# Optimization experiments

Measured on AMD Instinct MI355X. Metric: run time of the kernel, lower is better.

The kernel has to match this reference:

```python
import jax, jax.numpy as jnp
import numpy as np

H = 2048      # hidden_size
F = 1408      # moe_intermediate_size
E = 8         # num_experts
K = 2         # num_activated_experts
B, S = 4, 1024


def setup_inputs() -> dict:
    key = jax.random.key(0)
    ks = jax.random.split(key, 9)
    sc = 0.02
    return {
        "hidden_states": jax.random.normal(ks[0], (B, S, H), dtype=jnp.float32),
        "gate_w": jax.random.normal(ks[1], (E, H), dtype=jnp.float32) * sc,
        "bias": jnp.zeros((E,), dtype=jnp.float32),
        # shared expert (num_shared_experts = 1); torch Linear weight layout [out, in]
        "ws1": jax.random.normal(ks[2], (F, H), dtype=jnp.float32) * sc,
        "ws2": jax.random.normal(ks[3], (H, F), dtype=jnp.float32) * sc,
        "ws3": jax.random.normal(ks[4], (F, H), dtype=jnp.float32) * sc,
        # routed experts stacked along leading E axis
        "we1": jax.random.normal(ks[5], (E, F, H), dtype=jnp.float32) * sc,
        "we2": jax.random.normal(ks[6], (E, H, F), dtype=jnp.float32) * sc,
        "we3": jax.random.normal(ks[7], (E, F, H), dtype=jnp.float32) * sc,
    }


def reference(hidden_states, gate_w, bias, ws1, ws2, ws3, we1, we2, we3):
    orig_shape = hidden_states.shape
    x = hidden_states.reshape(-1, orig_shape[-1])      # [T, H]
    T = x.shape[0]

    # shared expert (SwiGLU)
    shared = (jax.nn.silu(x @ ws1.T) * (x @ ws3.T)) @ ws2.T   # [T, H]

    # sigmoid gating with bias-adjusted top-k selection
    scores = jax.nn.sigmoid(x @ gate_w.T)              # [T, E]
    routing_scores = scores + bias
    _, topk_idx = jax.lax.top_k(routing_scores, K)     # [T, K]
    sel = jnp.take_along_axis(scores, topk_idx, axis=1)
    gates = sel / sel.sum(axis=-1, keepdims=True)      # [T, K]

    # dense combine weights c[t, e] (top-k indices are distinct per token)
    c = jnp.zeros((T, E), dtype=x.dtype).at[jnp.arange(T)[:, None], topk_idx].add(gates)

    # all-expert SwiGLU, combined with sparse gate weights
    h1 = jnp.einsum("th,efh->etf", x, we1)             # [E, T, F]
    h3 = jnp.einsum("th,efh->etf", x, we3)
    act = jax.nn.silu(h1) * h3
    routed = jnp.einsum("etf,ehf,te->th", act, we2, c) # [T, H]

    return (shared + routed).reshape(orig_shape)
```

## Files before the change

kernel.cpp:

```cpp
#include <hip/hip_runtime.h>
#include <cstdint>
#include <cstddef>

#define TDIM 4096
#define HDIM 2048
#define FDIM 1408
#define NEXP 8
#define NSLOT (TDIM * 2)
#define BK 32

typedef _Float16 half8 __attribute__((ext_vector_type(8)));
typedef _Float16 half4 __attribute__((ext_vector_type(4)));
typedef float floatx4 __attribute__((ext_vector_type(4)));

#define AS1 __attribute__((address_space(1)))
#define AS3 __attribute__((address_space(3)))

__device__ __forceinline__ void g2l16(const _Float16* g, _Float16* l) {
  __builtin_amdgcn_global_load_lds((const AS1 unsigned*)g, (AS3 unsigned*)l, 16, 0, 0);
}

static constexpr size_t ws_align(size_t x) { return (x + 511) & ~(size_t)511; }
static constexpr size_t WS_XB     = 0;
static constexpr size_t WS_ACT_S  = WS_XB    + (size_t)TDIM * HDIM * 2;
static constexpr size_t WS_ACT_R  = WS_ACT_S + (size_t)TDIM * FDIM * 2;
static constexpr size_t WS_TOKE   = WS_ACT_R + (size_t)NSLOT * FDIM * 2;
static constexpr size_t WS_TOKG   = WS_TOKE  + (size_t)TDIM * 2 * 4;
static constexpr size_t WS_SLOTT  = WS_TOKG  + (size_t)TDIM * 2 * 4;
static constexpr size_t WS_SLOTG  = WS_SLOTT + (size_t)NSLOT * 4;
static constexpr size_t WS_COUNTS = WS_SLOTG + (size_t)NSLOT * 4;
static constexpr size_t WS_FILL   = WS_COUNTS + 64;
static constexpr size_t WS_OFFS   = WS_FILL   + 64;
static constexpr size_t WS_WS1H   = ws_align(WS_OFFS + 64);
static constexpr size_t WS_WS3H   = WS_WS1H + (size_t)FDIM * HDIM * 2;
static constexpr size_t WS_WS2H   = WS_WS3H + (size_t)FDIM * HDIM * 2;
static constexpr size_t WS_WE1H   = WS_WS2H + (size_t)HDIM * FDIM * 2;
static constexpr size_t WS_WE3H   = WS_WE1H + (size_t)NEXP * FDIM * HDIM * 2;
static constexpr size_t WS_WE2H   = WS_WE3H + (size_t)NEXP * FDIM * HDIM * 2;
static constexpr size_t WS_END    = WS_WE2H + (size_t)NEXP * HDIM * FDIM * 2;


__global__ void zero_meta_kernel(int* __restrict__ counts) {
  if (threadIdx.x < 32) counts[threadIdx.x] = 0;
}

__global__ void cvt3_kernel(const float* __restrict__ s0, const float* __restrict__ s1,
                            const float* __restrict__ s2, _Float16* __restrict__ d0,
                            _Float16* __restrict__ d1, _Float16* __restrict__ d2) {
  const float* s;
  _Float16* d;
  if (blockIdx.y == 0)      { s = s0; d = d0; }
  else if (blockIdx.y == 1) { s = s1; d = d1; }
  else                      { s = s2; d = d2; }
  size_t i = ((size_t)blockIdx.x * 256 + threadIdx.x) * 8;
  float4 a = *(const float4*)(s + i);
  float4 b = *(const float4*)(s + i + 4);
  half8 h;
  h[0] = (_Float16)a.x; h[1] = (_Float16)a.y; h[2] = (_Float16)a.z; h[3] = (_Float16)a.w;
  h[4] = (_Float16)b.x; h[5] = (_Float16)b.y; h[6] = (_Float16)b.z; h[7] = (_Float16)b.w;
  *(half8*)(d + i) = h;
}

__global__ void gate_kernel(const float* __restrict__ x, const float* __restrict__ gw,
                            const float* __restrict__ bias, _Float16* __restrict__ xb,
                            int* __restrict__ toke, float* __restrict__ tokg,
                            int* __restrict__ counts) {
  const int wid  = blockIdx.x * 4 + (threadIdx.x >> 6);
  const int lane = threadIdx.x & 63;
  const float4* xv = (const float4*)(x + (size_t)wid * HDIM);
  const float4* gv = (const float4*)gw;
  _Float16* xrow = xb + (size_t)wid * HDIM;
  float acc[NEXP];
#pragma unroll
  for (int e = 0; e < NEXP; ++e) acc[e] = 0.f;
#pragma unroll
  for (int i = 0; i < 8; ++i) {
    float4 xq = xv[lane + 64 * i];
    half4 hq;
    hq[0] = (_Float16)xq.x; hq[1] = (_Float16)xq.y;
    hq[2] = (_Float16)xq.z; hq[3] = (_Float16)xq.w;
    *(half4*)(xrow + 4 * (lane + 64 * i)) = hq;
#pragma unroll
    for (int e = 0; e < NEXP; ++e) {
      float4 gq = gv[e * 512 + lane + 64 * i];
      acc[e] += xq.x * gq.x + xq.y * gq.y + xq.z * gq.z + xq.w * gq.w;
    }
  }
#pragma unroll
  for (int e = 0; e < NEXP; ++e) {
    float v = acc[e];
    for (int off = 32; off; off >>= 1) v += __shfl_xor(v, off);
    acc[e] = v;
  }
  if (lane == 0) {
    float s[NEXP], r[NEXP];
#pragma unroll
    for (int e = 0; e < NEXP; ++e) {
      s[e] = 1.f / (1.f + __expf(-acc[e]));
      r[e] = s[e] + bias[e];
    }
    int e0 = 0;
#pragma unroll
    for (int e = 1; e < NEXP; ++e) if (r[e] > r[e0]) e0 = e;
    int e1 = -1;
#pragma unroll
    for (int e = 0; e < NEXP; ++e) if (e != e0 && (e1 < 0 || r[e] > r[e1])) e1 = e;
    float g0 = s[e0], g1 = s[e1];
    float inv = 1.f / (g0 + g1);
    toke[wid * 2]     = e0;
    toke[wid * 2 + 1] = e1;
    tokg[wid * 2]     = g0 * inv;
    tokg[wid * 2 + 1] = g1 * inv;
    atomicAdd(&counts[e0], 1);
    atomicAdd(&counts[e1], 1);
  }
}

__global__ void offsets_kernel(const int* __restrict__ counts, int* __restrict__ offs) {
  if (threadIdx.x == 0) {
    int o = 0;
    for (int e = 0; e < NEXP; ++e) { offs[e] = o; o += counts[e]; }
  }
}

__global__ void scatter_kernel(const int* __restrict__ toke, const float* __restrict__ tokg,
                               const int* __restrict__ offs, int* __restrict__ fill,
                               int* __restrict__ slott, float* __restrict__ slotg) {
  int t = blockIdx.x * 256 + threadIdx.x;
#pragma unroll
  for (int j = 0; j < 2; ++j) {
    int e = toke[t * 2 + j];
    float g = tokg[t * 2 + j];
    int p = offs[e] + atomicAdd(&fill[e], 1);
    slott[p] = t;
    slotg[p] = g;
  }
}


__global__ __launch_bounds__(256) void up_kernel(
    const _Float16* __restrict__ xb,
    const _Float16* __restrict__ ws1h, const _Float16* __restrict__ ws3h,
    const _Float16* __restrict__ we1h, const _Float16* __restrict__ we3h,
    _Float16* __restrict__ acts, _Float16* __restrict__ actr,
    const int* __restrict__ counts, const int* __restrict__ offs,
    const int* __restrict__ slott) {
  constexpr int GX = FDIM / 128;
  constexpr int GY = TDIM / 128;
  const int orig = blockIdx.x + GX * (blockIdx.y + GY * blockIdx.z);
  const int k8 = orig & 7, s = orig >> 3;
  const int g = k8 + 8 * (s / GX);
  const int lid = g * GX + (s % GX);
  const int bx = lid % GX;
  const int by = (lid / GX) % GY;
  const int bz = lid / (GX * GY);

  int cnt = TDIM, base = 0;
  const _Float16* __restrict__ W1 = ws1h;
  const _Float16* __restrict__ W3 = ws3h;
  _Float16* __restrict__ act = acts;
  bool gather = false;
  if (bz > 0) {
    const int e = bz - 1;
    cnt = counts[e];
    base = offs[e];
    if ((int)(by * 128) >= cnt) return;
    W1 = we1h + (size_t)e * FDIM * HDIM;
    W3 = we3h + (size_t)e * FDIM * HDIM;
    act = actr;
    gather = true;
  }
  const int m0 = by * 128, n0 = bx * 128;

  __shared__ _Float16 As[2][128 * BK];
  __shared__ _Float16 B1s[2][128 * BK];
  __shared__ _Float16 B3s[2][128 * BK];

  const int tid = threadIdx.x, lane = tid & 63, wv = tid >> 6;
  const int wm = wv >> 1, wn = wv & 1;
  const int lrow = lane & 15, quad = lane >> 4;

  const _Float16 *srcA[2], *srcB1[2], *srcB3[2];
#pragma unroll
  for (int j = 0; j < 2; ++j) {
    const int rr = wv * 32 + j * 16 + (lane >> 2);
    const int gc = ((lane & 3) ^ ((rr >> 1) & 3)) * 8;
    const int m = m0 + rr;
    int tok;
    if (gather) tok = slott[base + (m < cnt ? m : cnt - 1)];
    else tok = m;
    srcA[j]  = xb + (size_t)tok * HDIM + gc;
    srcB1[j] = W1 + (size_t)(n0 + rr) * HDIM + gc;
    srcB3[j] = W3 + (size_t)(n0 + rr) * HDIM + gc;
  }

  floatx4 acc1[4][4] = {};
  floatx4 acc3[4][4] = {};
  const int cA = (quad ^ ((lrow >> 1) & 3)) * 8;

#pragma unroll
  for (int j = 0; j < 2; ++j) {
    const int lb = (wv * 32 + j * 16) * BK;
    g2l16(srcA[j],  &As[0][lb]);
    g2l16(srcB1[j], &B1s[0][lb]);
    g2l16(srcB3[j], &B3s[0][lb]);
  }
  __syncthreads();

  for (int t = 0; t < HDIM / BK; ++t) {
    const int cur = t & 1;
    if (t + 1 < HDIM / BK) {
      const int k0 = (t + 1) * BK;
#pragma unroll
      for (int j = 0; j < 2; ++j) {
        const int lb = (wv * 32 + j * 16) * BK;
        g2l16(srcA[j] + k0,  &As[cur ^ 1][lb]);
        g2l16(srcB1[j] + k0, &B1s[cur ^ 1][lb]);
        g2l16(srcB3[j] + k0, &B3s[cur ^ 1][lb]);
      }
    }
    half8 af[4], b1f[4], b3f[4];
#pragma unroll
    for (int i = 0; i < 4; ++i)
      af[i] = *(const half8*)&As[cur][(wm * 64 + i * 16 + lrow) * BK + cA];
#pragma unroll
    for (int i = 0; i < 4; ++i) {
      b1f[i] = *(const half8*)&B1s[cur][(wn * 64 + i * 16 + lrow) * BK + cA];
      b3f[i] = *(const half8*)&B3s[cur][(wn * 64 + i * 16 + lrow) * BK + cA];
    }
#pragma unroll
    for (int ms = 0; ms < 4; ++ms)
#pragma unroll
      for (int ns = 0; ns < 4; ++ns) {
        acc1[ms][ns] = __builtin_amdgcn_mfma_f32_16x16x32_f16(af[ms], b1f[ns], acc1[ms][ns], 0, 0, 0);
        acc3[ms][ns] = __builtin_amdgcn_mfma_f32_16x16x32_f16(af[ms], b3f[ns], acc3[ms][ns], 0, 0, 0);
      }
    __syncthreads();
  }

#pragma unroll
  for (int ms = 0; ms < 4; ++ms)
#pragma unroll
    for (int ns = 0; ns < 4; ++ns)
#pragma unroll
      for (int r = 0; r < 4; ++r) {
        float h1 = acc1[ms][ns][r];
        float h3 = acc3[ms][ns][r];
        float a = h1 / (1.f + __expf(-h1)) * h3;
        const int rl = wm * 64 + ms * 16 + quad * 4 + r;
        const int f = n0 + wn * 64 + ns * 16 + lrow;
        const int m = m0 + rl;
        if (gather) {
          if (m < cnt) act[(size_t)(base + m) * FDIM + f] = (_Float16)a;
        } else {
          act[(size_t)m * FDIM + f] = (_Float16)a;
        }
      }
}

__global__ __launch_bounds__(256) void down_kernel(
    const _Float16* __restrict__ acts, const _Float16* __restrict__ actr,
    const _Float16* __restrict__ ws2h, const _Float16* __restrict__ we2h,
    float* __restrict__ out,
    const int* __restrict__ counts, const int* __restrict__ offs,
    const int* __restrict__ slott, const float* __restrict__ slotg) {
  constexpr int GX = HDIM / 128;
  constexpr int GY = TDIM / 128;
  const int orig = blockIdx.x + GX * (blockIdx.y + GY * blockIdx.z);
  const int k8 = orig & 7, s = orig >> 3;
  const int g = k8 + 8 * (s / GX);
  const int lid = g * GX + (s % GX);
  const int bx = lid % GX;
  const int by = (lid / GX) % GY;
  const int bz = lid / (GX * GY);

  int cnt = TDIM, base = 0;
  const _Float16* __restrict__ A = acts;
  const _Float16* __restrict__ W = ws2h;
  bool gather = false;
  if (bz > 0) {
    const int e = bz - 1;
    cnt = counts[e];
    base = offs[e];
    if ((int)(by * 128) >= cnt) return;
    A = actr;
    W = we2h + (size_t)e * HDIM * FDIM;
    gather = true;
  }
  const int m0 = by * 128, n0 = bx * 128;

  __shared__ _Float16 As[2][128 * BK];
  __shared__ _Float16 Bs[2][128 * BK];

  const int tid = threadIdx.x, lane = tid & 63, wv = tid >> 6;
  const int wm = wv >> 1, wn = wv & 1;
  const int lrow = lane & 15, quad = lane >> 4;

  const _Float16 *srcA[2], *srcB[2];
#pragma unroll
  for (int j = 0; j < 2; ++j) {
    const int rr = wv * 32 + j * 16 + (lane >> 2);
    const int gc = ((lane & 3) ^ ((rr >> 1) & 3)) * 8;
    const int m = m0 + rr;
    int srow;
    if (gather) srow = base + (m < cnt ? m : cnt - 1);
    else srow = m;
    srcA[j] = A + (size_t)srow * FDIM + gc;
    srcB[j] = W + (size_t)(n0 + rr) * FDIM + gc;
  }

  floatx4 acc[4][4] = {};
  const int cA = (quad ^ ((lrow >> 1) & 3)) * 8;

#pragma unroll
  for (int j = 0; j < 2; ++j) {
    const int lb = (wv * 32 + j * 16) * BK;
    g2l16(srcA[j], &As[0][lb]);
    g2l16(srcB[j], &Bs[0][lb]);
  }
  __syncthreads();

  for (int t = 0; t < FDIM / BK; ++t) {
    const int cur = t & 1;
    if (t + 1 < FDIM / BK) {
      const int k0 = (t + 1) * BK;
#pragma unroll
      for (int j = 0; j < 2; ++j) {
        const int lb = (wv * 32 + j * 16) * BK;
        g2l16(srcA[j] + k0, &As[cur ^ 1][lb]);
        g2l16(srcB[j] + k0, &Bs[cur ^ 1][lb]);
      }
    }
    half8 af[4], bf[4];
#pragma unroll
    for (int i = 0; i < 4; ++i)
      af[i] = *(const half8*)&As[cur][(wm * 64 + i * 16 + lrow) * BK + cA];
#pragma unroll
    for (int i = 0; i < 4; ++i)
      bf[i] = *(const half8*)&Bs[cur][(wn * 64 + i * 16 + lrow) * BK + cA];
#pragma unroll
    for (int ms = 0; ms < 4; ++ms)
#pragma unroll
      for (int ns = 0; ns < 4; ++ns)
        acc[ms][ns] = __builtin_amdgcn_mfma_f32_16x16x32_f16(af[ms], bf[ns], acc[ms][ns], 0, 0, 0);
    __syncthreads();
  }

#pragma unroll
  for (int ms = 0; ms < 4; ++ms)
#pragma unroll
    for (int ns = 0; ns < 4; ++ns)
#pragma unroll
      for (int r = 0; r < 4; ++r) {
        float v = acc[ms][ns][r];
        const int rl = wm * 64 + ms * 16 + quad * 4 + r;
        const int h = n0 + wn * 64 + ns * 16 + lrow;
        const int m = m0 + rl;
        if (gather) {
          if (m < cnt) {
            const int sl = base + m;
            atomicAdd(&out[(size_t)slott[sl] * HDIM + h], v * slotg[sl]);
          }
        } else {
          atomicAdd(&out[(size_t)m * HDIM + h], v);
        }
      }
}


extern "C" void kernel_launch(void* const* d_in, const int* in_sizes, int n_in,
                              void* d_out, int out_size, void* d_ws, size_t ws_size,
                              hipStream_t stream) {
  const float* x    = (const float*)d_in[0];
  const float* gw   = (const float*)d_in[1];
  const float* bias = (const float*)d_in[2];
  const float* ws1  = (const float*)d_in[3];
  const float* ws2  = (const float*)d_in[4];
  const float* ws3  = (const float*)d_in[5];
  const float* we1  = (const float*)d_in[6];
  const float* we2  = (const float*)d_in[7];
  const float* we3  = (const float*)d_in[8];
  float* out = (float*)d_out;

  char* ws = (char*)d_ws;
  _Float16* xb   = (_Float16*)(ws + WS_XB);
  _Float16* acts = (_Float16*)(ws + WS_ACT_S);
  _Float16* actr = (_Float16*)(ws + WS_ACT_R);
  int*   toke  = (int*)(ws + WS_TOKE);
  float* tokg  = (float*)(ws + WS_TOKG);
  int*   slott = (int*)(ws + WS_SLOTT);
  float* slotg = (float*)(ws + WS_SLOTG);
  int* counts  = (int*)(ws + WS_COUNTS);
  int* fill    = (int*)(ws + WS_FILL);
  int* offs    = (int*)(ws + WS_OFFS);
  _Float16* ws1h = (_Float16*)(ws + WS_WS1H);
  _Float16* ws3h = (_Float16*)(ws + WS_WS3H);
  _Float16* ws2h = (_Float16*)(ws + WS_WS2H);
  _Float16* we1h = (_Float16*)(ws + WS_WE1H);
  _Float16* we3h = (_Float16*)(ws + WS_WE3H);
  _Float16* we2h = (_Float16*)(ws + WS_WE2H);

  hipLaunchKernelGGL(zero_meta_kernel, dim3(1), dim3(64), 0, stream, counts);
  hipLaunchKernelGGL(gate_kernel, dim3(1024), dim3(256), 0, stream, x, gw, bias, xb, toke, tokg, counts);
  hipLaunchKernelGGL(offsets_kernel, dim3(1), dim3(64), 0, stream, counts, offs);
  hipLaunchKernelGGL(scatter_kernel, dim3(16), dim3(256), 0, stream, toke, tokg, offs, fill, slott, slotg);

  constexpr int GS = (FDIM * HDIM) / 2048;
  constexpr int GR = (NEXP * FDIM * HDIM) / 2048;
  hipLaunchKernelGGL(cvt3_kernel, dim3(GS, 3), dim3(256), 0, stream, ws1, ws3, ws2, ws1h, ws3h, ws2h);
  hipLaunchKernelGGL(cvt3_kernel, dim3(GR, 3), dim3(256), 0, stream, we1, we3, we2, we1h, we3h, we2h);

  hipMemsetAsync(out, 0, (size_t)TDIM * HDIM * sizeof(float), stream);

  hipLaunchKernelGGL(up_kernel, dim3(FDIM / 128, TDIM / 128, NEXP + 1), dim3(256), 0, stream,
                     xb, ws1h, ws3h, we1h, we3h, acts, actr, counts, offs, slott);
  hipLaunchKernelGGL(down_kernel, dim3(HDIM / 128, TDIM / 128, NEXP + 1), dim3(256), 0, stream,
                     acts, actr, ws2h, we2h, out, counts, offs, slott, slotg);
}
```

Baseline: 966.7 us.

## Split fused up-projection GEMM and replace down atomics with a merge pass

```diff
diff --git a/kernel.cpp b/kernel.cpp
--- a/kernel.cpp
+++ b/kernel.cpp
@@ -28,7 +28,8 @@
 static constexpr size_t WS_TOKG   = WS_TOKE  + (size_t)TDIM * 2 * 4;
 static constexpr size_t WS_SLOTT  = WS_TOKG  + (size_t)TDIM * 2 * 4;
 static constexpr size_t WS_SLOTG  = WS_SLOTT + (size_t)NSLOT * 4;
-static constexpr size_t WS_COUNTS = WS_SLOTG + (size_t)NSLOT * 4;
+static constexpr size_t WS_TOKS   = WS_SLOTG + (size_t)NSLOT * 4;
+static constexpr size_t WS_COUNTS = WS_TOKS  + (size_t)TDIM * 2 * 4;
 static constexpr size_t WS_FILL   = WS_COUNTS + 64;
 static constexpr size_t WS_OFFS   = WS_FILL   + 64;
 static constexpr size_t WS_WS1H   = ws_align(WS_OFFS + 64);
@@ -37,7 +38,10 @@
 static constexpr size_t WS_WE1H   = WS_WS2H + (size_t)HDIM * FDIM * 2;
 static constexpr size_t WS_WE3H   = WS_WE1H + (size_t)NEXP * FDIM * HDIM * 2;
 static constexpr size_t WS_WE2H   = WS_WE3H + (size_t)NEXP * FDIM * HDIM * 2;
-static constexpr size_t WS_END    = WS_WE2H + (size_t)NEXP * HDIM * FDIM * 2;
+static constexpr size_t WS_H1S    = WS_WE2H + (size_t)NEXP * HDIM * FDIM * 2;
+static constexpr size_t WS_H1R    = WS_H1S + (size_t)TDIM * FDIM * 2;
+static constexpr size_t WS_RB     = WS_H1R + (size_t)NSLOT * FDIM * 2;
+static constexpr size_t WS_END    = WS_RB + (size_t)NSLOT * HDIM * 2;
 
 
 __global__ void zero_meta_kernel(int* __restrict__ counts) {
@@ -125,7 +129,8 @@
 
 __global__ void scatter_kernel(const int* __restrict__ toke, const float* __restrict__ tokg,
                                const int* __restrict__ offs, int* __restrict__ fill,
-                               int* __restrict__ slott, float* __restrict__ slotg) {
+                               int* __restrict__ slott, float* __restrict__ slotg,
+                               int* __restrict__ tokslot) {
   int t = blockIdx.x * 256 + threadIdx.x;
 #pragma unroll
   for (int j = 0; j < 2; ++j) {
@@ -134,15 +139,17 @@
     int p = offs[e] + atomicAdd(&fill[e], 1);
     slott[p] = t;
     slotg[p] = g;
-  }
-}
-
-
-__global__ __launch_bounds__(256) void up_kernel(
+    tokslot[t * 2 + j] = p;
+  }
+}
+
+
+template <bool FIN>
+__global__ __launch_bounds__(256) void up_gemm(
     const _Float16* __restrict__ xb,
-    const _Float16* __restrict__ ws1h, const _Float16* __restrict__ ws3h,
-    const _Float16* __restrict__ we1h, const _Float16* __restrict__ we3h,
-    _Float16* __restrict__ acts, _Float16* __restrict__ actr,
+    const _Float16* __restrict__ wsh, const _Float16* __restrict__ weh,
+    _Float16* __restrict__ dsts, _Float16* __restrict__ dstr,
+    const _Float16* __restrict__ h1s, const _Float16* __restrict__ h1r,
     const int* __restrict__ counts, const int* __restrict__ offs,
     const int* __restrict__ slott) {
   constexpr int GX = FDIM / 128;
@@ -156,31 +163,30 @@
   const int bz = lid / (GX * GY);
 
   int cnt = TDIM, base = 0;
-  const _Float16* __restrict__ W1 = ws1h;
-  const _Float16* __restrict__ W3 = ws3h;
-  _Float16* __restrict__ act = acts;
+  const _Float16* __restrict__ W = wsh;
+  _Float16* __restrict__ dst = dsts;
+  const _Float16* __restrict__ h1 = h1s;
   bool gather = false;
   if (bz > 0) {
     const int e = bz - 1;
     cnt = counts[e];
     base = offs[e];
     if ((int)(by * 128) >= cnt) return;
-    W1 = we1h + (size_t)e * FDIM * HDIM;
-    W3 = we3h + (size_t)e * FDIM * HDIM;
-    act = actr;
+    W = weh + (size_t)e * FDIM * HDIM;
+    dst = dstr;
+    h1 = h1r;
     gather = true;
   }
   const int m0 = by * 128, n0 = bx * 128;
 
   __shared__ _Float16 As[2][128 * BK];
-  __shared__ _Float16 B1s[2][128 * BK];
-  __shared__ _Float16 B3s[2][128 * BK];
+  __shared__ _Float16 Bs[2][128 * BK];
 
   const int tid = threadIdx.x, lane = tid & 63, wv = tid >> 6;
   const int wm = wv >> 1, wn = wv & 1;
   const int lrow = lane & 15, quad = lane >> 4;
 
-  const _Float16 *srcA[2], *srcB1[2], *srcB3[2];
+  const _Float16 *srcA[2], *srcB[2];
 #pragma unroll
   for (int j = 0; j < 2; ++j) {
     const int rr = wv * 32 + j * 16 + (lane >> 2);
@@ -189,21 +195,18 @@
     int tok;
     if (gather) tok = slott[base + (m < cnt ? m : cnt - 1)];
     else tok = m;
-    srcA[j]  = xb + (size_t)tok * HDIM + gc;
-    srcB1[j] = W1 + (size_t)(n0 + rr) * HDIM + gc;
-    srcB3[j] = W3 + (size_t)(n0 + rr) * HDIM + gc;
-  }
-
-  floatx4 acc1[4][4] = {};
-  floatx4 acc3[4][4] = {};
+    srcA[j] = xb + (size_t)tok * HDIM + gc;
+    srcB[j] = W + (size_t)(n0 + rr) * HDIM + gc;
+  }
+
+  floatx4 acc[4][4] = {};
   const int cA = (quad ^ ((lrow >> 1) & 3)) * 8;
 
 #pragma unroll
   for (int j = 0; j < 2; ++j) {
     const int lb = (wv * 32 + j * 16) * BK;
-    g2l16(srcA[j],  &As[0][lb]);
-    g2l16(srcB1[j], &B1s[0][lb]);
-    g2l16(srcB3[j], &B3s[0][lb]);
+    g2l16(srcA[j], &As[0][lb]);
+    g2l16(srcB[j], &Bs[0][lb]);
   }
   __syncthreads();
 
@@ -214,27 +217,22 @@
 #pragma unroll
       for (int j = 0; j < 2; ++j) {
         const int lb = (wv * 32 + j * 16) * BK;
-        g2l16(srcA[j] + k0,  &As[cur ^ 1][lb]);
-        g2l16(srcB1[j] + k0, &B1s[cur ^ 1][lb]);
-        g2l16(srcB3[j] + k0, &B3s[cur ^ 1][lb]);
+        g2l16(srcA[j] + k0, &As[cur ^ 1][lb]);
+        g2l16(srcB[j] + k0, &Bs[cur ^ 1][lb]);
       }
     }
-    half8 af[4], b1f[4], b3f[4];
+    half8 af[4], bf[4];
 #pragma unroll
     for (int i = 0; i < 4; ++i)
       af[i] = *(const half8*)&As[cur][(wm * 64 + i * 16 + lrow) * BK + cA];
 #pragma unroll
-    for (int i = 0; i < 4; ++i) {
-      b1f[i] = *(const half8*)&B1s[cur][(wn * 64 + i * 16 + lrow) * BK + cA];
-      b3f[i] = *(const half8*)&B3s[cur][(wn * 64 + i * 16 + lrow) * BK + cA];
-    }
+    for (int i = 0; i < 4; ++i)
+      bf[i] = *(const half8*)&Bs[cur][(wn * 64 + i * 16 + lrow) * BK + cA];
 #pragma unroll
     for (int ms = 0; ms < 4; ++ms)
 #pragma unroll
-      for (int ns = 0; ns < 4; ++ns) {
-        acc1[ms][ns] = __builtin_amdgcn_mfma_f32_16x16x32_f16(af[ms], b1f[ns], acc1[ms][ns], 0, 0, 0);
-        acc3[ms][ns] = __builtin_amdgcn_mfma_f32_16x16x32_f16(af[ms], b3f[ns], acc3[ms][ns], 0, 0, 0);
-      }
+      for (int ns = 0; ns < 4; ++ns)
+        acc[ms][ns] = __builtin_amdgcn_mfma_f32_16x16x32_f16(af[ms], bf[ns], acc[ms][ns], 0, 0, 0);
     __syncthreads();
   }
 
@@ -244,16 +242,18 @@
     for (int ns = 0; ns < 4; ++ns)
 #pragma unroll
       for (int r = 0; r < 4; ++r) {
-        float h1 = acc1[ms][ns][r];
-        float h3 = acc3[ms][ns][r];
-        float a = h1 / (1.f + __expf(-h1)) * h3;
         const int rl = wm * 64 + ms * 16 + quad * 4 + r;
         const int f = n0 + wn * 64 + ns * 16 + lrow;
         const int m = m0 + rl;
-        if (gather) {
-          if (m < cnt) act[(size_t)(base + m) * FDIM + f] = (_Float16)a;
+        if (gather && m >= cnt) continue;
+        const size_t row = gather ? (size_t)(base + m) : (size_t)m;
+        float v = acc[ms][ns][r];
+        if constexpr (FIN) {
+          float h = (float)h1[row * FDIM + f];
+          float a = h / (1.f + __expf(-h)) * v;
+          dst[row * FDIM + f] = (_Float16)a;
         } else {
-          act[(size_t)m * FDIM + f] = (_Float16)a;
+          dst[row * FDIM + f] = (_Float16)v;
         }
       }
 }
@@ -261,9 +261,8 @@
 __global__ __launch_bounds__(256) void down_kernel(
     const _Float16* __restrict__ acts, const _Float16* __restrict__ actr,
     const _Float16* __restrict__ ws2h, const _Float16* __restrict__ we2h,
-    float* __restrict__ out,
-    const int* __restrict__ counts, const int* __restrict__ offs,
-    const int* __restrict__ slott, const float* __restrict__ slotg) {
+    float* __restrict__ out, _Float16* __restrict__ rbuf,
+    const int* __restrict__ counts, const int* __restrict__ offs) {
   constexpr int GX = HDIM / 128;
   constexpr int GY = TDIM / 128;
   const int orig = blockIdx.x + GX * (blockIdx.y + GY * blockIdx.z);
@@ -357,14 +356,34 @@
         const int h = n0 + wn * 64 + ns * 16 + lrow;
         const int m = m0 + rl;
         if (gather) {
-          if (m < cnt) {
-            const int sl = base + m;
-            atomicAdd(&out[(size_t)slott[sl] * HDIM + h], v * slotg[sl]);
-          }
+          if (m < cnt) rbuf[(size_t)(base + m) * HDIM + h] = (_Float16)v;
         } else {
-          atomicAdd(&out[(size_t)m * HDIM + h], v);
+          out[(size_t)m * HDIM + h] = v;
         }
       }
+}
+
+__global__ void merge_kernel(float* __restrict__ out, const _Float16* __restrict__ rbuf,
+                             const int* __restrict__ tokslot, const float* __restrict__ tokg) {
+  const int t = blockIdx.x;
+  const int hc = threadIdx.x * 8;
+  const int p0 = tokslot[t * 2], p1 = tokslot[t * 2 + 1];
+  const float g0 = tokg[t * 2], g1 = tokg[t * 2 + 1];
+  half8 r0 = *(const half8*)(rbuf + (size_t)p0 * HDIM + hc);
+  half8 r1 = *(const half8*)(rbuf + (size_t)p1 * HDIM + hc);
+  float* o = out + (size_t)t * HDIM + hc;
+  float4 a = *(float4*)o;
+  float4 b = *(float4*)(o + 4);
+  a.x += g0 * (float)r0[0] + g1 * (float)r1[0];
+  a.y += g0 * (float)r0[1] + g1 * (float)r1[1];
+  a.z += g0 * (float)r0[2] + g1 * (float)r1[2];
+  a.w += g0 * (float)r0[3] + g1 * (float)r1[3];
+  b.x += g0 * (float)r0[4] + g1 * (float)r1[4];
+  b.y += g0 * (float)r0[5] + g1 * (float)r1[5];
+  b.z += g0 * (float)r0[6] + g1 * (float)r1[6];
+  b.w += g0 * (float)r0[7] + g1 * (float)r1[7];
+  *(float4*)o = a;
+  *(float4*)(o + 4) = b;
 }
 
 
@@ -390,6 +409,7 @@
   float* tokg  = (float*)(ws + WS_TOKG);
   int*   slott = (int*)(ws + WS_SLOTT);
   float* slotg = (float*)(ws + WS_SLOTG);
+  int*   toks  = (int*)(ws + WS_TOKS);
   int* counts  = (int*)(ws + WS_COUNTS);
   int* fill    = (int*)(ws + WS_FILL);
   int* offs    = (int*)(ws + WS_OFFS);
@@ -399,21 +419,25 @@
   _Float16* we1h = (_Float16*)(ws + WS_WE1H);
   _Float16* we3h = (_Float16*)(ws + WS_WE3H);
   _Float16* we2h = (_Float16*)(ws + WS_WE2H);
+  _Float16* h1s  = (_Float16*)(ws + WS_H1S);
+  _Float16* h1r  = (_Float16*)(ws + WS_H1R);
+  _Float16* rbuf = (_Float16*)(ws + WS_RB);
 
   hipLaunchKernelGGL(zero_meta_kernel, dim3(1), dim3(64), 0, stream, counts);
   hipLaunchKernelGGL(gate_kernel, dim3(1024), dim3(256), 0, stream, x, gw, bias, xb, toke, tokg, counts);
   hipLaunchKernelGGL(offsets_kernel, dim3(1), dim3(64), 0, stream, counts, offs);
-  hipLaunchKernelGGL(scatter_kernel, dim3(16), dim3(256), 0, stream, toke, tokg, offs, fill, slott, slotg);
+  hipLaunchKernelGGL(scatter_kernel, dim3(16), dim3(256), 0, stream, toke, tokg, offs, fill, slott, slotg, toks);
 
   constexpr int GS = (FDIM * HDIM) / 2048;
   constexpr int GR = (NEXP * FDIM * HDIM) / 2048;
   hipLaunchKernelGGL(cvt3_kernel, dim3(GS, 3), dim3(256), 0, stream, ws1, ws3, ws2, ws1h, ws3h, ws2h);
   hipLaunchKernelGGL(cvt3_kernel, dim3(GR, 3), dim3(256), 0, stream, we1, we3, we2, we1h, we3h, we2h);
 
-  hipMemsetAsync(out, 0, (size_t)TDIM * HDIM * sizeof(float), stream);
-
-  hipLaunchKernelGGL(up_kernel, dim3(FDIM / 128, TDIM / 128, NEXP + 1), dim3(256), 0, stream,
-                     xb, ws1h, ws3h, we1h, we3h, acts, actr, counts, offs, slott);
+  hipLaunchKernelGGL((up_gemm<false>), dim3(FDIM / 128, TDIM / 128, NEXP + 1), dim3(256), 0, stream,
+                     xb, ws1h, we1h, h1s, h1r, nullptr, nullptr, counts, offs, slott);
+  hipLaunchKernelGGL((up_gemm<true>), dim3(FDIM / 128, TDIM / 128, NEXP + 1), dim3(256), 0, stream,
+                     xb, ws3h, we3h, acts, actr, h1s, h1r, counts, offs, slott);
   hipLaunchKernelGGL(down_kernel, dim3(HDIM / 128, TDIM / 128, NEXP + 1), dim3(256), 0, stream,
-                     acts, actr, ws2h, we2h, out, counts, offs, slott, slotg);
-}
+                     acts, actr, ws2h, we2h, out, rbuf, counts, offs);
+  hipLaunchKernelGGL(merge_kernel, dim3(TDIM), dim3(256), 0, stream, out, rbuf, toks, tokg);
+}
```

Result: faster. 912.8 us (-5.6%).
